# Performance work log

Hardware: AMD Instinct MI355X
Metric: run time of the kernel (lower is better)

Reference implementation:

```python
import jax, jax.numpy as jnp
import numpy as np


def setup_inputs() -> dict:
    key = jax.random.key(0)
    k1, k2, k3, k4 = jax.random.split(key, 4)
    B, C, T, H, W = 2, 64, 8, 48, 48
    C2 = C // 2
    x_in = jax.random.normal(k1, (B, C, T, H, W), dtype=jnp.float32)
    # per-time-slice 1x1 conv weights (theta/phi pairs), kaiming-ish scale
    theta_w = jax.random.normal(k2, (T, C2, C), dtype=jnp.float32) / np.sqrt(C)
    phi_w = jax.random.normal(k3, (T, C2, C), dtype=jnp.float32) / np.sqrt(C)
    out_w = jax.random.normal(k4, (C, C), dtype=jnp.float32) / np.sqrt(C)
    return {"x_in": x_in, "theta_w": theta_w, "phi_w": phi_w, "out_w": out_w}


def reference(x_in, theta_w, phi_w, out_w):
    B, C, T, H, W = x_in.shape
    C2 = theta_w.shape[1]
    P = H * W
    # [B, T, C, P] layout: flatten spatial, move time next to batch
    x = jnp.transpose(x_in, (0, 2, 1, 3, 4)).reshape(B, T, C, P)
    # per-slice 1x1 convs == per-slice channel matmuls with slice-specific weights
    theta = jnp.einsum("toc,btcp->btop", theta_w, x)  # [B,T,C2,P]
    phi = jnp.einsum("toc,btcp->btop", phi_w, x)      # [B,T,C2,P]
    scale = 1.0 / jnp.sqrt(jnp.asarray(C2, dtype=x_in.dtype))
    scores = jnp.einsum("btcp,btcq->btpq", theta, phi) * scale  # [B,T,P,P]
    attn = jax.nn.softmax(scores, axis=-1)
    f = jnp.einsum("btpq,btcq->btcp", attn, x)  # value = raw x, [B,T,C,P]
    # conv_out: 1x1x1 Conv3d (pointwise over channels), then residual
    out = jnp.einsum("oc,btcp->btop", out_w, f)
    out = jnp.transpose(out.reshape(B, T, C, H, W), (0, 2, 1, 3, 4))
    return out + x_in
```

## Files before the change

### kernel.cpp

```cpp
#include <hip/hip_runtime.h>
#include <hip/hip_bf16.h>

#define CC 64
#define TT 8
#define PP 2304
#define C2 32
#define BT 16
#define NKT 36
#define HKT 18
#define SCALE2 0.25503486f

using h8 = __attribute__((ext_vector_type(8))) _Float16;
using h4 = __attribute__((ext_vector_type(4))) _Float16;
using f4 = __attribute__((ext_vector_type(4))) float;

#if __has_builtin(__builtin_amdgcn_exp2f)
#define EXP2(v) __builtin_amdgcn_exp2f(v)
#else
#define EXP2(v) exp2f(v)
#endif

#define SWIZ_BT(xcd, g) ((xcd) + 8 * ((g) & 1))
#define SWIZ_PT(g) ((g) >> 1)


__global__ __launch_bounds__(256) void k_prep(
    const float* __restrict__ x, const float* __restrict__ tw,
    const float* __restrict__ pw, _Float16* __restrict__ thf,
    _Float16* __restrict__ rec) {
  const int qt = SWIZ_PT(blockIdx.y), bt = SWIZ_BT(blockIdx.x, blockIdx.y);
  const int b = bt >> 3, t = bt & 7;
  const int tid = threadIdx.x;
  const int wv = tid >> 6, lane = tid & 63;
  const int quad = lane >> 4, l15 = lane & 15;

  __shared__ __align__(16) float x_s[64][68];
  __shared__ __align__(16) _Float16 th_s[4][16][32];
  __shared__ __align__(16) _Float16 ph_s[4][16][32];

  const size_t xslice = ((size_t)b * CC * TT + t) * PP;
  const int qg0 = qt * 64;

  {
    const int qq = tid & 63;
    const int c0 = (tid >> 6) * 16;
#pragma unroll
    for (int i = 0; i < 16; i++) {
      int c = c0 + i;
      x_s[qq][c] = x[xslice + (size_t)c * (TT * PP) + qg0 + qq];
    }
  }
  __syncthreads();

  h8 bx[2];
#pragma unroll
  for (int ks = 0; ks < 2; ks++) {
    const float* row = &x_s[wv * 16 + l15][ks * 32 + quad * 8];
    float4 u0 = *reinterpret_cast<const float4*>(row);
    float4 u1 = *reinterpret_cast<const float4*>(row + 4);
    bx[ks][0] = (_Float16)u0.x; bx[ks][1] = (_Float16)u0.y;
    bx[ks][2] = (_Float16)u0.z; bx[ks][3] = (_Float16)u0.w;
    bx[ks][4] = (_Float16)u1.x; bx[ks][5] = (_Float16)u1.y;
    bx[ks][6] = (_Float16)u1.z; bx[ks][7] = (_Float16)u1.w;
  }

  const float* twt = tw + t * C2 * CC;
  const float* pwt = pw + t * C2 * CC;
  const f4 zero = {0.f, 0.f, 0.f, 0.f};
  f4 accT[2] = {zero, zero}, accP[2] = {zero, zero};
#pragma unroll
  for (int mt = 0; mt < 2; mt++)
#pragma unroll
    for (int ks = 0; ks < 2; ks++) {
      const float* wr = twt + (mt * 16 + l15) * CC + ks * 32 + quad * 8;
      const float* pr = pwt + (mt * 16 + l15) * CC + ks * 32 + quad * 8;
      float4 a0 = *reinterpret_cast<const float4*>(wr);
      float4 a1 = *reinterpret_cast<const float4*>(wr + 4);
      float4 p0 = *reinterpret_cast<const float4*>(pr);
      float4 p1 = *reinterpret_cast<const float4*>(pr + 4);
      h8 at = {(_Float16)a0.x, (_Float16)a0.y, (_Float16)a0.z, (_Float16)a0.w,
               (_Float16)a1.x, (_Float16)a1.y, (_Float16)a1.z, (_Float16)a1.w};
      h8 ap = {(_Float16)p0.x, (_Float16)p0.y, (_Float16)p0.z, (_Float16)p0.w,
               (_Float16)p1.x, (_Float16)p1.y, (_Float16)p1.z, (_Float16)p1.w};
      accT[mt] =
          __builtin_amdgcn_mfma_f32_16x16x32_f16(at, bx[ks], accT[mt], 0, 0, 0);
      accP[mt] =
          __builtin_amdgcn_mfma_f32_16x16x32_f16(ap, bx[ks], accP[mt], 0, 0, 0);
    }

#pragma unroll
  for (int mt = 0; mt < 2; mt++) {
    h4 tv, pv;
#pragma unroll
    for (int r = 0; r < 4; r++) {
      tv[r] = (_Float16)(accT[mt][r] * SCALE2);
      pv[r] = (_Float16)accP[mt][r];
    }
    *reinterpret_cast<h4*>(&th_s[wv][l15][mt * 16 + quad * 4]) = tv;
    *reinterpret_cast<h4*>(&ph_s[wv][l15][mt * 16 + quad * 4]) = pv;
  }

  h8 tfrag = *reinterpret_cast<const h8*>(&th_s[wv][l15][quad * 8]);
  *reinterpret_cast<h8*>(
      thf + (((size_t)(bt * NKT + qt) * 4 + wv) * 64 + lane) * 8) = tfrag;

  _Float16* rb = rec + (size_t)(bt * NKT + qt) * 6144;
  h8 pfrag = *reinterpret_cast<const h8*>(&ph_s[wv][l15][quad * 8]);
  *reinterpret_cast<h8*>(rb + wv * 512 + lane * 8) = pfrag;

#pragma unroll
  for (int ctp = 0; ctp < 2; ctp++) {
    h8 v;
#pragma unroll
    for (int j = 0; j < 4; j++) {
      v[j] = (_Float16)x_s[wv * 16 + quad * 4 + j][(2 * ctp) * 16 + l15];
      v[4 + j] = (_Float16)x_s[wv * 16 + quad * 4 + j][(2 * ctp + 1) * 16 + l15];
    }
    *reinterpret_cast<h8*>(rb + 2048 + (wv * 2 + ctp) * 512 + lane * 8) = v;
  }
}

__global__ __launch_bounds__(256, 3) void k_attn(
    const float* __restrict__ x, const _Float16* __restrict__ thf,
    const _Float16* __restrict__ rec, const float* __restrict__ ow,
    float* __restrict__ out) {
  const int pt = SWIZ_PT(blockIdx.y), bt = SWIZ_BT(blockIdx.x, blockIdx.y);
  const int b = bt >> 3, t = bt & 7;
  const int tid = threadIdx.x;
  const int wv = tid >> 6, lane = tid & 63;
  const int quad = lane >> 4, l15 = lane & 15;
  const int qg = wv & 1, kg = wv >> 1;

  __shared__ __align__(16) float exch[4 * 17 * 64];
  __shared__ __align__(16) float out_s[64 * 68];

  h8 b_th[2];
#pragma unroll
  for (int ps = 0; ps < 2; ps++)
    b_th[ps] = *reinterpret_cast<const h8*>(
        thf + (((size_t)(bt * NKT + pt) * 4 + qg * 2 + ps) * 64 + lane) * 8);

  const _Float16* mybase =
      rec + ((size_t)bt * NKT + (size_t)kg * HKT) * 6144 + lane * 8;

  int4 cur[12], nxt[12];
#pragma unroll
  for (int j = 0; j < 12; j++)
    cur[j] = *reinterpret_cast<const int4*>(mybase + j * 512);

  const f4 zero = {0.f, 0.f, 0.f, 0.f};
  f4 O[2][4] = {{zero, zero, zero, zero}, {zero, zero, zero, zero}};
  float l_sum[2] = {0.f, 0.f};

  for (int i = 0; i < HKT; i++) {
    if (i < HKT - 1) {
      const _Float16* nb = mybase + (size_t)(i + 1) * 6144;
#pragma unroll
      for (int j = 0; j < 12; j++)
        nxt[j] = *reinterpret_cast<const int4*>(nb + j * 512);
    }

    f4 s[4][2];
#pragma unroll
    for (int nt = 0; nt < 4; nt++) {
      h8 aphi = *reinterpret_cast<const h8*>(&cur[nt]);
#pragma unroll
      for (int ps = 0; ps < 2; ps++)
        s[nt][ps] = __builtin_amdgcn_mfma_f32_16x16x32_f16(aphi, b_th[ps],
                                                           zero, 0, 0, 0);
    }

#pragma unroll
    for (int nt = 0; nt < 4; nt++) {
      h4 bw[2];
#pragma unroll
      for (int ps = 0; ps < 2; ps++)
#pragma unroll
        for (int r = 0; r < 4; r++) {
          float w = EXP2(s[nt][ps][r]);
          l_sum[ps] += w;
          bw[ps][r] = (_Float16)w;
        }
#pragma unroll
      for (int ctp = 0; ctp < 2; ctp++) {
        h8 xx = *reinterpret_cast<const h8*>(&cur[4 + nt * 2 + ctp]);
        h4 a0 = __builtin_shufflevector(xx, xx, 0, 1, 2, 3);
        h4 a1 = __builtin_shufflevector(xx, xx, 4, 5, 6, 7);
#pragma unroll
        for (int ps = 0; ps < 2; ps++) {
          O[ps][2 * ctp] = __builtin_amdgcn_mfma_f32_16x16x16f16(
              a0, bw[ps], O[ps][2 * ctp], 0, 0, 0);
          O[ps][2 * ctp + 1] = __builtin_amdgcn_mfma_f32_16x16x16f16(
              a1, bw[ps], O[ps][2 * ctp + 1], 0, 0, 0);
        }
      }
    }

    if (i < HKT - 1) {
#pragma unroll
      for (int j = 0; j < 12; j++) cur[j] = nxt[j];
    }
  }

#pragma unroll
  for (int ps = 0; ps < 2; ps++) {
    l_sum[ps] += __shfl_xor(l_sum[ps], 16);
    l_sum[ps] += __shfl_xor(l_sum[ps], 32);
  }

  if (kg == 1) {
#pragma unroll
    for (int ps = 0; ps < 2; ps++) {
#pragma unroll
      for (int k = 0; k < 16; k++)
        exch[((qg * 2 + ps) * 17 + k) * 64 + lane] = O[ps][k >> 2][k & 3];
      exch[((qg * 2 + ps) * 17 + 16) * 64 + lane] = l_sum[ps];
    }
  }
  __syncthreads();

  if (kg == 0) {
#pragma unroll
    for (int ps = 0; ps < 2; ps++) {
#pragma unroll
      for (int k = 0; k < 16; k++)
        O[ps][k >> 2][k & 3] += exch[((qg * 2 + ps) * 17 + k) * 64 + lane];
      const float inv =
          1.f / (l_sum[ps] + exch[((qg * 2 + ps) * 17 + 16) * 64 + lane]);

      h4 bf[4];
#pragma unroll
      for (int ct = 0; ct < 4; ct++)
#pragma unroll
        for (int r = 0; r < 4; r++) bf[ct][r] = (_Float16)(O[ps][ct][r] * inv);

      f4 D3[4] = {zero, zero, zero, zero};
#pragma unroll
      for (int mt = 0; mt < 4; mt++)
#pragma unroll
        for (int ct = 0; ct < 4; ct++) {
          const float* wrow =
              ow + (size_t)(mt * 16 + l15) * CC + ct * 16 + quad * 4;
          float4 u = *reinterpret_cast<const float4*>(wrow);
          h4 aw = {(_Float16)u.x, (_Float16)u.y, (_Float16)u.z, (_Float16)u.w};
          D3[mt] =
              __builtin_amdgcn_mfma_f32_16x16x16f16(aw, bf[ct], D3[mt], 0, 0, 0);
        }

#pragma unroll
      for (int mt = 0; mt < 4; mt++)
#pragma unroll
        for (int r = 0; r < 4; r++)
          out_s[(mt * 16 + quad * 4 + r) * 68 + (qg * 2 + ps) * 16 + l15] =
              D3[mt][r];
    }
  }
  __syncthreads();

  const int co = tid >> 2;
  const int psub = (tid & 3) * 16;
  const size_t gbase = ((size_t)(b * CC + co) * TT + t) * PP + pt * 64 + psub;
#pragma unroll
  for (int jj = 0; jj < 4; jj++) {
    float4 vo =
        *reinterpret_cast<const float4*>(&out_s[co * 68 + psub + jj * 4]);
    float4 xr = *reinterpret_cast<const float4*>(&x[gbase + jj * 4]);
    vo.x += xr.x; vo.y += xr.y; vo.z += xr.z; vo.w += xr.w;
    *reinterpret_cast<float4*>(&out[gbase + jj * 4]) = vo;
  }
}

extern "C" void kernel_launch(void* const* d_in, const int* in_sizes, int n_in,
                              void* d_out, int out_size, void* d_ws,
                              size_t ws_size, hipStream_t stream) {
  (void)in_sizes; (void)n_in; (void)out_size; (void)ws_size;
  const float* x = (const float*)d_in[0];
  const float* tw = (const float*)d_in[1];
  const float* pw = (const float*)d_in[2];
  const float* ow = (const float*)d_in[3];
  float* out = (float*)d_out;

  _Float16* thf = (_Float16*)d_ws;
  _Float16* rec = thf + (size_t)BT * NKT * 4 * 64 * 8;

  k_prep<<<dim3(8, 72), 256, 0, stream>>>(x, tw, pw, thf, rec);
  k_attn<<<dim3(8, 72), 256, 0, stream>>>(x, thf, rec, ow, out);
}
```

Baseline: 110.3 us.

## Split attention across four key groups per block with 32-query tiles

Each attention block now covers 32 queries instead of 64, and its four waves split the key range into quarters instead of two query groups by two key halves. The grid doubles to 1152 blocks and launch bounds allow 4 blocks per CU, with a three-way cross-wave reduction through shared memory. This aims to raise parallelism and occupancy and shorten the per-wave serial key loop. The cost is that each key/value tile is streamed from global memory twice as often, and the epilogue does more reduction work relative to the output it produces.

```diff
diff --git a/kernel.cpp b/kernel.cpp
--- a/kernel.cpp
+++ b/kernel.cpp
@@ -7,7 +7,7 @@
 #define C2 32
 #define BT 16
 #define NKT 36
-#define HKT 18
+#define QKT 9
 #define SCALE2 0.25503486f
 
 using h8 = __attribute__((ext_vector_type(8))) _Float16;
@@ -21,14 +21,14 @@
 #endif
 
 #define SWIZ_BT(xcd, g) ((xcd) + 8 * ((g) & 1))
-#define SWIZ_PT(g) ((g) >> 1)
+#define SWIZ_G(g) ((g) >> 1)
 
 
 __global__ __launch_bounds__(256) void k_prep(
     const float* __restrict__ x, const float* __restrict__ tw,
     const float* __restrict__ pw, _Float16* __restrict__ thf,
     _Float16* __restrict__ rec) {
-  const int qt = SWIZ_PT(blockIdx.y), bt = SWIZ_BT(blockIdx.x, blockIdx.y);
+  const int qt = SWIZ_G(blockIdx.y), bt = SWIZ_BT(blockIdx.x, blockIdx.y);
   const int b = bt >> 3, t = bt & 7;
   const int tid = threadIdx.x;
   const int wv = tid >> 6, lane = tid & 63;
@@ -120,28 +120,27 @@
   }
 }
 
-__global__ __launch_bounds__(256, 3) void k_attn(
+__global__ __launch_bounds__(256, 4) void k_attn(
     const float* __restrict__ x, const _Float16* __restrict__ thf,
     const _Float16* __restrict__ rec, const float* __restrict__ ow,
     float* __restrict__ out) {
-  const int pt = SWIZ_PT(blockIdx.y), bt = SWIZ_BT(blockIdx.x, blockIdx.y);
+  const int pt32 = SWIZ_G(blockIdx.y), bt = SWIZ_BT(blockIdx.x, blockIdx.y);
   const int b = bt >> 3, t = bt & 7;
   const int tid = threadIdx.x;
-  const int wv = tid >> 6, lane = tid & 63;
+  const int kg = tid >> 6, lane = tid & 63;
   const int quad = lane >> 4, l15 = lane & 15;
-  const int qg = wv & 1, kg = wv >> 1;
-
-  __shared__ __align__(16) float exch[4 * 17 * 64];
-  __shared__ __align__(16) float out_s[64 * 68];
+
+  __shared__ __align__(16) float exch[3 * 2 * 17 * 64];
+  __shared__ __align__(16) float out_s[64 * 36];
 
   h8 b_th[2];
 #pragma unroll
   for (int ps = 0; ps < 2; ps++)
     b_th[ps] = *reinterpret_cast<const h8*>(
-        thf + (((size_t)(bt * NKT + pt) * 4 + qg * 2 + ps) * 64 + lane) * 8);
+        thf + (((size_t)bt * (NKT * 4) + pt32 * 2 + ps) * 64 + lane) * 8);
 
   const _Float16* mybase =
-      rec + ((size_t)bt * NKT + (size_t)kg * HKT) * 6144 + lane * 8;
+      rec + ((size_t)bt * NKT + (size_t)kg * QKT) * 6144 + lane * 8;
 
   int4 cur[12], nxt[12];
 #pragma unroll
@@ -152,8 +151,8 @@
   f4 O[2][4] = {{zero, zero, zero, zero}, {zero, zero, zero, zero}};
   float l_sum[2] = {0.f, 0.f};
 
-  for (int i = 0; i < HKT; i++) {
-    if (i < HKT - 1) {
+  for (int i = 0; i < QKT; i++) {
+    if (i < QKT - 1) {
       const _Float16* nb = mybase + (size_t)(i + 1) * 6144;
 #pragma unroll
       for (int j = 0; j < 12; j++)
@@ -196,7 +195,7 @@
       }
     }
 
-    if (i < HKT - 1) {
+    if (i < QKT - 1) {
 #pragma unroll
       for (int j = 0; j < 12; j++) cur[j] = nxt[j];
     }
@@ -208,13 +207,13 @@
     l_sum[ps] += __shfl_xor(l_sum[ps], 32);
   }
 
-  if (kg == 1) {
+  if (kg > 0) {
 #pragma unroll
     for (int ps = 0; ps < 2; ps++) {
 #pragma unroll
       for (int k = 0; k < 16; k++)
-        exch[((qg * 2 + ps) * 17 + k) * 64 + lane] = O[ps][k >> 2][k & 3];
-      exch[((qg * 2 + ps) * 17 + 16) * 64 + lane] = l_sum[ps];
+        exch[(((kg - 1) * 2 + ps) * 17 + k) * 64 + lane] = O[ps][k >> 2][k & 3];
+      exch[(((kg - 1) * 2 + ps) * 17 + 16) * 64 + lane] = l_sum[ps];
     }
   }
   __syncthreads();
@@ -222,11 +221,15 @@
   if (kg == 0) {
 #pragma unroll
     for (int ps = 0; ps < 2; ps++) {
-#pragma unroll
-      for (int k = 0; k < 16; k++)
-        O[ps][k >> 2][k & 3] += exch[((qg * 2 + ps) * 17 + k) * 64 + lane];
-      const float inv =
-          1.f / (l_sum[ps] + exch[((qg * 2 + ps) * 17 + 16) * 64 + lane]);
+      float lt = l_sum[ps];
+#pragma unroll
+      for (int g = 0; g < 3; g++) {
+#pragma unroll
+        for (int k = 0; k < 16; k++)
+          O[ps][k >> 2][k & 3] += exch[((g * 2 + ps) * 17 + k) * 64 + lane];
+        lt += exch[((g * 2 + ps) * 17 + 16) * 64 + lane];
+      }
+      const float inv = 1.f / lt;
 
       h4 bf[4];
 #pragma unroll
@@ -251,19 +254,19 @@
       for (int mt = 0; mt < 4; mt++)
 #pragma unroll
         for (int r = 0; r < 4; r++)
-          out_s[(mt * 16 + quad * 4 + r) * 68 + (qg * 2 + ps) * 16 + l15] =
-              D3[mt][r];
+          out_s[(mt * 16 + quad * 4 + r) * 36 + ps * 16 + l15] = D3[mt][r];
     }
   }
   __syncthreads();
 
   const int co = tid >> 2;
-  const int psub = (tid & 3) * 16;
-  const size_t gbase = ((size_t)(b * CC + co) * TT + t) * PP + pt * 64 + psub;
-#pragma unroll
-  for (int jj = 0; jj < 4; jj++) {
+  const int psub = (tid & 3) * 8;
+  const size_t gbase =
+      ((size_t)(b * CC + co) * TT + t) * PP + pt32 * 32 + psub;
+#pragma unroll
+  for (int jj = 0; jj < 2; jj++) {
     float4 vo =
-        *reinterpret_cast<const float4*>(&out_s[co * 68 + psub + jj * 4]);
+        *reinterpret_cast<const float4*>(&out_s[co * 36 + psub + jj * 4]);
     float4 xr = *reinterpret_cast<const float4*>(&x[gbase + jj * 4]);
     vo.x += xr.x; vo.y += xr.y; vo.z += xr.z; vo.w += xr.w;
     *reinterpret_cast<float4*>(&out[gbase + jj * 4]) = vo;
@@ -284,5 +287,5 @@
   _Float16* rec = thf + (size_t)BT * NKT * 4 * 64 * 8;
 
   k_prep<<<dim3(8, 72), 256, 0, stream>>>(x, tw, pw, thf, rec);
-  k_attn<<<dim3(8, 72), 256, 0, stream>>>(x, thf, rec, ow, out);
+  k_attn<<<dim3(8, 144), 256, 0, stream>>>(x, thf, rec, ow, out);
 }
```

After: 116.0 us. +5.2%, slower.
